# Kernel tuning notes

Measured on AMD Instinct MI355X. Metric: run time of the kernel, lower is better.

The kernel has to match this reference:

```python
import jax, jax.numpy as jnp
import numpy as np
import math

IN_DIM = 1024
OUT_DIM = 1024
GRID_SIZE = 5
SPLINE_ORDER = 3
N_COEFFS = GRID_SIZE + SPLINE_ORDER          # 8
N_KNOTS = GRID_SIZE + 2 * SPLINE_ORDER + 1   # 12
EPS = 1e-08


def setup_inputs() -> dict:
    key = jax.random.key(0)
    k_x, k_c, k_w = jax.random.split(key, 3)
    B = 4096
    x = jax.random.normal(k_x, (B, IN_DIM), dtype=jnp.float32)
    coeffs = jax.random.normal(k_c, (OUT_DIM, IN_DIM * N_COEFFS), dtype=jnp.float32) * 0.1
    # kaiming_uniform(a=sqrt(5)) -> U(-bound, bound), bound = sqrt(6/((1+a^2)*fan_in)) = 1/sqrt(fan_in)
    bound = 1.0 / math.sqrt(IN_DIM)
    base_weight = jax.random.uniform(k_w, (OUT_DIM, IN_DIM), dtype=jnp.float32,
                                     minval=-bound, maxval=bound)
    step = 2.0 / GRID_SIZE
    init_val = math.log(math.exp(step) - 1.0)
    grid_steps_log = jnp.full((IN_DIM, N_KNOTS - 1), init_val, dtype=jnp.float32)
    grid_start = jnp.full((IN_DIM, 1), -1.0 - SPLINE_ORDER * step, dtype=jnp.float32)
    res_scale = jnp.zeros((1,), dtype=jnp.float32)
    return {"x": x, "coeffs": coeffs, "base_weight": base_weight,
            "grid_steps_log": grid_steps_log, "grid_start": grid_start,
            "res_scale": res_scale}


def _get_grid(grid_steps_log, grid_start):
    steps = jax.nn.softplus(grid_steps_log)            # [in, n_knots-1]
    grid = jnp.concatenate([grid_start, steps], axis=-1)
    return jnp.cumsum(grid, axis=-1)                   # [in, n_knots]


def _b_spline(x, grid):
    # x: [B, in], grid: [in, n_knots] -> bases: [B, in, n_coeffs]
    x_u = x[:, :, None]                                # [B, in, 1]
    g = grid[None, :, :]                               # [1, in, n_knots]
    bases = ((x_u >= g[:, :, :-1]) & (x_u < g[:, :, 1:])).astype(x.dtype)
    for d in range(1, SPLINE_ORDER + 1):
        left = (x_u - g[:, :, :-(d + 1)]) / (g[:, :, d:-1] - g[:, :, :-(d + 1)] + EPS)
        right = (g[:, :, d + 1:] - x_u) / (g[:, :, d + 1:] - g[:, :, 1:-d] + EPS)
        bases = left * bases[:, :, :-1] + right * bases[:, :, 1:]
    return bases


def reference(x, coeffs, base_weight, grid_steps_log, grid_start, res_scale):
    grid = _get_grid(grid_steps_log, grid_start)
    spline_basis = _b_spline(x, grid)                  # [B, in, n_coeffs]
    B = spline_basis.shape[0]
    spline_flat = spline_basis.reshape(B, -1)          # [B, in*n_coeffs]
    spline_out = spline_flat @ coeffs.T                # [B, out]
    base_out = jax.nn.silu(x) @ base_weight.T          # [B, out]
    y = spline_out + base_out
    y = y + res_scale * x                              # residual (in_dim == out_dim)
    return y
```

## Files before the change

kernel.cpp:

```cpp
#include <hip/hip_runtime.h>

#define IN_DIM   1024
#define OUT_DIM  1024
#define BATCH    4096
#define NC       8
#define NK       12
#define KSPLINE  (IN_DIM * NC)
#define KDIM     (KSPLINE + IN_DIM)
#define EPS      1e-8f

#define NBLK_A   ((IN_DIM / 256) * (BATCH / 16))
#define NBLK_W   ((OUT_DIM * (KDIM / 4)) / 256)

#define BM       256
#define BN       128
#define BKQ      32
#define KSPLIT   2
#define KPS      (KDIM / KSPLIT)
#define NKT      (KPS / BKQ)
#define NGBLK    ((BATCH / BM) * (OUT_DIM / BN) * KSPLIT)

#define SWZ(r)   (((r) >> 1) & 3)

typedef _Float16 f16x8  __attribute__((ext_vector_type(8)));
typedef float    f32x4  __attribute__((ext_vector_type(4)));

static __device__ __forceinline__ unsigned short f2h_bits(float f) {
  _Float16 h = (_Float16)f;
  return __builtin_bit_cast(unsigned short, h);
}

static __device__ __forceinline__ void gl_lds16(const unsigned short* g, unsigned short* l) {
  __builtin_amdgcn_global_load_lds(
      (const __attribute__((address_space(1))) unsigned int*)g,
      (__attribute__((address_space(3))) unsigned int*)l, 16, 0, 0);
}

__global__ __launch_bounds__(256) void prep_k(const float* __restrict__ x,
                                              const float* __restrict__ coeffs,
                                              const float* __restrict__ bw,
                                              const float* __restrict__ gsl,
                                              const float* __restrict__ gstart,
                                              const float* __restrict__ rsp,
                                              unsigned short* __restrict__ A,
                                              unsigned short* __restrict__ W,
                                              float* __restrict__ out) {
  const int blk = blockIdx.x;
  if (blk < NBLK_A) {
    const int i  = (blk & 3) * 256 + threadIdx.x;
    const int b0 = (blk >> 2) * 16;
    const float rs = rsp[0];
    float g[NK];
    float acc = gstart[i];
    g[0] = acc;
#pragma unroll
    for (int t = 0; t < NK - 1; ++t) {
      float v  = gsl[i * (NK - 1) + t];
      float sp = (v > 20.f) ? v : log1pf(expf(v));
      acc += sp;
      g[t + 1] = acc;
    }
    float r[30];
#pragma unroll
    for (int j = 0; j < 11; ++j) r[j]      = 1.f / (g[j + 1] - g[j] + EPS);
#pragma unroll
    for (int j = 0; j < 10; ++j) r[11 + j] = 1.f / (g[j + 2] - g[j] + EPS);
#pragma unroll
    for (int j = 0; j <  9; ++j) r[21 + j] = 1.f / (g[j + 3] - g[j] + EPS);

#pragma unroll 4
    for (int bb = 0; bb < 16; ++bb) {
      const int b = b0 + bb;
      float xv = x[(size_t)b * IN_DIM + i];
      float bas[NK - 1];
#pragma unroll
      for (int k = 0; k < NK - 1; ++k)
        bas[k] = (xv >= g[k] && xv < g[k + 1]) ? 1.f : 0.f;
      const int off[3] = {0, 11, 21};
#pragma unroll
      for (int d = 1; d <= 3; ++d) {
#pragma unroll
        for (int k = 0; k < NK - 1 - d; ++k) {
          float left  = (xv - g[k])         * r[off[d - 1] + k];
          float right = (g[k + d + 1] - xv) * r[off[d - 1] + k + 1];
          bas[k] = left * bas[k] + right * bas[k + 1];
        }
      }
      uint4 pack;
      pack.x = (unsigned)f2h_bits(bas[0]) | ((unsigned)f2h_bits(bas[1]) << 16);
      pack.y = (unsigned)f2h_bits(bas[2]) | ((unsigned)f2h_bits(bas[3]) << 16);
      pack.z = (unsigned)f2h_bits(bas[4]) | ((unsigned)f2h_bits(bas[5]) << 16);
      pack.w = (unsigned)f2h_bits(bas[6]) | ((unsigned)f2h_bits(bas[7]) << 16);
      *(uint4*)&A[(size_t)b * KDIM + i * NC] = pack;
      float s = xv / (1.f + expf(-xv));
      A[(size_t)b * KDIM + KSPLINE + i] = f2h_bits(s);
      out[(size_t)b * OUT_DIM + i] = rs * xv;
    }
  } else {
    int idx = (blk - NBLK_A) * 256 + threadIdx.x;
    int n  = idx / (KDIM / 4);
    int k4 = (idx - n * (KDIM / 4)) * 4;
    float4 v;
    if (k4 < KSPLINE) v = *(const float4*)&coeffs[(size_t)n * KSPLINE + k4];
    else              v = *(const float4*)&bw[(size_t)n * IN_DIM + (k4 - KSPLINE)];
    ushort4 o;
    o.x = f2h_bits(v.x); o.y = f2h_bits(v.y); o.z = f2h_bits(v.z); o.w = f2h_bits(v.w);
    *(ushort4*)&W[(size_t)n * KDIM + k4] = o;
  }
}

__global__ __launch_bounds__(512, 2) void gemm_k(const unsigned short* __restrict__ A,
                                                 const unsigned short* __restrict__ W,
                                                 float* __restrict__ out,
                                                 float* __restrict__ P,
                                                 int use_partial) {
  __shared__ __align__(16) unsigned short As[4][BM][BKQ];
  __shared__ __align__(16) unsigned short Bs[4][BN][BKQ];
  const int tid  = threadIdx.x;
  const int wave = tid >> 6;
  const int lane = tid & 63;

  const int s  = (blockIdx.x & 7) * 32 + (blockIdx.x >> 3);
  const int ks = s >> 7;
  const int bn = (s >> 4) & 7;
  const int bm = s & 15;

  const int srow = tid >> 2;
  const int scsw = ((tid & 3) ^ SWZ(srow)) * 8;
  const unsigned short* aG = A + (size_t)(bm * BM + srow) * KDIM + (size_t)ks * KPS + scsw;
  const unsigned short* bG = W + (size_t)(bn * BN + srow) * KDIM + (size_t)ks * KPS + scsw;

#define STAGE(t) do {                                                          \
    const int sl_ = (t) & 3; const int kb_ = (t) * BKQ;                        \
    gl_lds16(aG + kb_,                      &As[sl_][wave * 16][0]);           \
    gl_lds16(aG + (size_t)128 * KDIM + kb_, &As[sl_][128 + wave * 16][0]);     \
    gl_lds16(bG + kb_,                      &Bs[sl_][wave * 16][0]);           \
  } while (0)

  const int l15 = lane & 15;
  const int kg  = lane >> 4;
  const int wm  = (wave >> 1) * 64;
  const int wn  = (wave & 1) * 64;

  f32x4 acc[4][4] = {};

  STAGE(0); STAGE(1); STAGE(2);
  asm volatile("s_waitcnt vmcnt(6)" ::: "memory");
  __builtin_amdgcn_s_barrier();

#pragma unroll 4
  for (int kt = 0; kt < NKT; ++kt) {
    const unsigned short* as = &As[kt & 3][0][0];
    const unsigned short* bs = &Bs[kt & 3][0][0];
    f16x8 af[4], bf[4];
#pragma unroll
    for (int mt = 0; mt < 4; ++mt) {
      int row = wm + mt * 16 + l15;
      af[mt] = *(const f16x8*)&as[row * BKQ + ((kg ^ SWZ(row)) * 8)];
    }
#pragma unroll
    for (int nt = 0; nt < 4; ++nt) {
      int row = wn + nt * 16 + l15;
      bf[nt] = *(const f16x8*)&bs[row * BKQ + ((kg ^ SWZ(row)) * 8)];
    }
    if (kt < NKT - 3) STAGE(kt + 3);
    __builtin_amdgcn_s_setprio(1);
#pragma unroll
    for (int mt = 0; mt < 4; ++mt)
#pragma unroll
      for (int nt = 0; nt < 4; ++nt)
        acc[mt][nt] = __builtin_amdgcn_mfma_f32_16x16x32_f16(af[mt], bf[nt], acc[mt][nt], 0, 0, 0);
    __builtin_amdgcn_s_setprio(0);
    if (kt < NKT - 3)       asm volatile("s_waitcnt vmcnt(6)" ::: "memory");
    else if (kt == NKT - 3) asm volatile("s_waitcnt vmcnt(3)" ::: "memory");
    else if (kt == NKT - 2) asm volatile("s_waitcnt vmcnt(0)" ::: "memory");
    if (kt < NKT - 1) __builtin_amdgcn_s_barrier();
  }
#undef STAGE

#pragma unroll
  for (int mt = 0; mt < 4; ++mt) {
#pragma unroll
    for (int reg = 0; reg < 4; ++reg) {
      const int row = bm * BM + wm + mt * 16 + kg * 4 + reg;
      const size_t ro = (size_t)row * OUT_DIM;
#pragma unroll
      for (int nt = 0; nt < 4; ++nt) {
        const int col = bn * BN + wn + nt * 16 + l15;
        const float v = acc[mt][nt][reg];
        if (use_partial) {
          if (ks == 0) out[ro + col] += v;
          else         P[ro + col]    = v;
        } else {
          atomicAdd(&out[ro + col], v);
        }
      }
    }
  }
}

__global__ __launch_bounds__(256) void reduce_k(float* __restrict__ out,
                                                const float* __restrict__ P) {
  const int n4 = (BATCH * OUT_DIM) / 4;
  for (int i = blockIdx.x * 256 + threadIdx.x; i < n4; i += gridDim.x * 256) {
    float4 o = ((const float4*)out)[i];
    float4 p = ((const float4*)P)[i];
    o.x += p.x; o.y += p.y; o.z += p.z; o.w += p.w;
    ((float4*)out)[i] = o;
  }
}

extern "C" void kernel_launch(void* const* d_in, const int* in_sizes, int n_in,
                              void* d_out, int out_size, void* d_ws, size_t ws_size,
                              hipStream_t stream) {
  const float* x      = (const float*)d_in[0];
  const float* coeffs = (const float*)d_in[1];
  const float* bw     = (const float*)d_in[2];
  const float* gsl    = (const float*)d_in[3];
  const float* gstart = (const float*)d_in[4];
  const float* rsp    = (const float*)d_in[5];

  const size_t szA = (size_t)BATCH * KDIM * 2;
  const size_t szW = (size_t)OUT_DIM * KDIM * 2;
  const size_t szP = (size_t)BATCH * OUT_DIM * 4;
  char* ws = (char*)d_ws;
  unsigned short* A  = (unsigned short*)ws;
  unsigned short* W  = (unsigned short*)(ws + szA);
  float*          P  = (float*)(ws + szA + szW);
  float*          out = (float*)d_out;
  const int use_partial = (ws_size >= szA + szW + szP) ? 1 : 0;

  prep_k<<<NBLK_A + NBLK_W, 256, 0, stream>>>(x, coeffs, bw, gsl, gstart, rsp, A, W, out);
  gemm_k<<<NGBLK, 512, 0, stream>>>(A, W, out, P, use_partial);
  if (use_partial) reduce_k<<<2048, 256, 0, stream>>>(out, P);
}
```

Baseline: 241.4 us.

## Restructure GEMM mainloop with BK=64, half-tile staging and interleaved MFMA phases

Doubles the K-tile to 64 and splits each A/B tile into half-tiles held in a 6-slot LDS ring. Each K step is broken into two phases, each running LDS fragment loads, prefetch of the next half-tiles and a batch of MFMAs, separated by barriers. The per-wave layout changes from a 64x64 wave tile to 128x32, and the XOR swizzle is widened to 8 chunks. Launch bounds drop to one block per CU, trading occupancy for a deeper, more finely interleaved load/compute pipeline. The loop runs in groups of three tiles, which assumes NKT is a multiple of three.

```diff
diff --git a/kernel.cpp b/kernel.cpp
--- a/kernel.cpp
+++ b/kernel.cpp
@@ -14,13 +14,13 @@
 
 #define BM       256
 #define BN       128
-#define BKQ      32
+#define BK       64
 #define KSPLIT   2
 #define KPS      (KDIM / KSPLIT)
-#define NKT      (KPS / BKQ)
+#define NKT      (KPS / BK)
 #define NGBLK    ((BATCH / BM) * (OUT_DIM / BN) * KSPLIT)
 
-#define SWZ(r)   (((r) >> 1) & 3)
+#define SWZ(r)   ((r) & 7)
 
 typedef _Float16 f16x8  __attribute__((ext_vector_type(8)));
 typedef float    f32x4  __attribute__((ext_vector_type(4)));
@@ -109,13 +109,13 @@
   }
 }
 
-__global__ __launch_bounds__(512, 2) void gemm_k(const unsigned short* __restrict__ A,
+__global__ __launch_bounds__(512, 1) void gemm_k(const unsigned short* __restrict__ A,
                                                  const unsigned short* __restrict__ W,
                                                  float* __restrict__ out,
                                                  float* __restrict__ P,
                                                  int use_partial) {
-  __shared__ __align__(16) unsigned short As[4][BM][BKQ];
-  __shared__ __align__(16) unsigned short Bs[4][BN][BKQ];
+  __shared__ __align__(16) unsigned short Al[6][128][64];
+  __shared__ __align__(16) unsigned short Bl[6][64][64];
   const int tid  = threadIdx.x;
   const int wave = tid >> 6;
   const int lane = tid & 63;
@@ -125,68 +125,112 @@
   const int bn = (s >> 4) & 7;
   const int bm = s & 15;
 
-  const int srow = tid >> 2;
-  const int scsw = ((tid & 3) ^ SWZ(srow)) * 8;
+  const int srow = tid >> 3;
+  const int scsw = ((tid & 7) ^ SWZ(srow)) * 8;
   const unsigned short* aG = A + (size_t)(bm * BM + srow) * KDIM + (size_t)ks * KPS + scsw;
   const unsigned short* bG = W + (size_t)(bn * BN + srow) * KDIM + (size_t)ks * KPS + scsw;
 
-#define STAGE(t) do {                                                          \
-    const int sl_ = (t) & 3; const int kb_ = (t) * BKQ;                        \
-    gl_lds16(aG + kb_,                      &As[sl_][wave * 16][0]);           \
-    gl_lds16(aG + (size_t)128 * KDIM + kb_, &As[sl_][128 + wave * 16][0]);     \
-    gl_lds16(bG + kb_,                      &Bs[sl_][wave * 16][0]);           \
+#define STAGE_A(u, sl, h) do {                                                 \
+    const size_t k_ = (size_t)(u) * BK;                                        \
+    gl_lds16(aG + ((size_t)(h) * 128)      * KDIM + k_, &Al[sl][wave * 8][0]); \
+    gl_lds16(aG + ((size_t)(h) * 128 + 64) * KDIM + k_, &Al[sl][64 + wave * 8][0]); \
   } while (0)
+#define STAGE_B(u, sl, h)                                                      \
+    gl_lds16(bG + ((size_t)(h) * 64) * KDIM + (size_t)(u) * BK, &Bl[sl][wave * 8][0])
 
   const int l15 = lane & 15;
   const int kg  = lane >> 4;
-  const int wm  = (wave >> 1) * 64;
-  const int wn  = (wave & 1) * 64;
-
-  f32x4 acc[4][4] = {};
-
-  STAGE(0); STAGE(1); STAGE(2);
+  const int wm  = (wave >> 2) * 128;
+  const int hA  = wave >> 2;
+  const int hB  = (wave & 3) >> 1;
+  const int wnl = (wave & 1) * 32;
+
+  f32x4 acc[8][2] = {};
+  f16x8 af[4][2], bf[2][2];
+
+  auto LDA = [&](const unsigned short (*As_)[64], int qm) {
+#pragma unroll
+    for (int i = 0; i < 4; ++i) {
+      const int rh = qm * 64 + i * 16 + l15;
+      const int sw = SWZ(rh);
+#pragma unroll
+      for (int kc = 0; kc < 2; ++kc)
+        af[i][kc] = *(const f16x8*)&As_[rh][((kc * 4 + kg) ^ sw) * 8];
+    }
+  };
+  auto LDB = [&](const unsigned short (*Bs_)[64]) {
+#pragma unroll
+    for (int j = 0; j < 2; ++j) {
+      const int rh = wnl + j * 16 + l15;
+      const int sw = SWZ(rh);
+#pragma unroll
+      for (int kc = 0; kc < 2; ++kc)
+        bf[j][kc] = *(const f16x8*)&Bs_[rh][((kc * 4 + kg) ^ sw) * 8];
+    }
+  };
+  auto MFMA_Q = [&](int m0) {
+#pragma unroll
+    for (int kc = 0; kc < 2; ++kc)
+#pragma unroll
+      for (int i = 0; i < 4; ++i)
+#pragma unroll
+        for (int j = 0; j < 2; ++j)
+          acc[m0 + i][j] = __builtin_amdgcn_mfma_f32_16x16x32_f16(af[i][kc], bf[j][kc], acc[m0 + i][j], 0, 0, 0);
+  };
+
+  STAGE_A(0, 0, 0); STAGE_B(0, 0, 0); STAGE_A(0, 1, 1); STAGE_B(0, 1, 1);
+  STAGE_A(1, 2, 0); STAGE_B(1, 2, 0); STAGE_A(1, 3, 1); STAGE_B(1, 3, 1);
   asm volatile("s_waitcnt vmcnt(6)" ::: "memory");
   __builtin_amdgcn_s_barrier();
 
-#pragma unroll 4
-  for (int kt = 0; kt < NKT; ++kt) {
-    const unsigned short* as = &As[kt & 3][0][0];
-    const unsigned short* bs = &Bs[kt & 3][0][0];
-    f16x8 af[4], bf[4];
-#pragma unroll
-    for (int mt = 0; mt < 4; ++mt) {
-      int row = wm + mt * 16 + l15;
-      af[mt] = *(const f16x8*)&as[row * BKQ + ((kg ^ SWZ(row)) * 8)];
-    }
-#pragma unroll
-    for (int nt = 0; nt < 4; ++nt) {
-      int row = wn + nt * 16 + l15;
-      bf[nt] = *(const f16x8*)&bs[row * BKQ + ((kg ^ SWZ(row)) * 8)];
-    }
-    if (kt < NKT - 3) STAGE(kt + 3);
-    __builtin_amdgcn_s_setprio(1);
-#pragma unroll
-    for (int mt = 0; mt < 4; ++mt)
-#pragma unroll
-      for (int nt = 0; nt < 4; ++nt)
-        acc[mt][nt] = __builtin_amdgcn_mfma_f32_16x16x32_f16(af[mt], bf[nt], acc[mt][nt], 0, 0, 0);
-    __builtin_amdgcn_s_setprio(0);
-    if (kt < NKT - 3)       asm volatile("s_waitcnt vmcnt(6)" ::: "memory");
-    else if (kt == NKT - 3) asm volatile("s_waitcnt vmcnt(3)" ::: "memory");
-    else if (kt == NKT - 2) asm volatile("s_waitcnt vmcnt(0)" ::: "memory");
-    if (kt < NKT - 1) __builtin_amdgcn_s_barrier();
-  }
-#undef STAGE
-
-#pragma unroll
-  for (int mt = 0; mt < 4; ++mt) {
+#define TILE(u, S0) do {                                                       \
+    const unsigned short (*As_)[64] = Al[(S0) + hA];                           \
+    const unsigned short (*Bs_)[64] = Bl[(S0) + hB];                           \
+                   \
+    LDA(As_, 0); LDB(Bs_);                                                     \
+    if ((u) + 2 < NKT) { STAGE_A((u) + 2, ((S0) + 4) % 6, 0);                  \
+                         STAGE_B((u) + 2, ((S0) + 4) % 6, 0); }                \
+    __builtin_amdgcn_s_barrier();                                              \
+    asm volatile("s_waitcnt lgkmcnt(0)" ::: "memory");                         \
+    __builtin_amdgcn_sched_barrier(0);                                         \
+    __builtin_amdgcn_s_setprio(1);                                             \
+    MFMA_Q(0);                                                                 \
+    __builtin_amdgcn_s_setprio(0);                                             \
+    __builtin_amdgcn_s_barrier();                                              \
+       \
+    LDA(As_, 1);                                                               \
+    if ((u) + 2 < NKT) { STAGE_A((u) + 2, ((S0) + 5) % 6, 1);                  \
+                         STAGE_B((u) + 2, ((S0) + 5) % 6, 1); }                \
+    __builtin_amdgcn_s_barrier();                                              \
+    asm volatile("s_waitcnt lgkmcnt(0)" ::: "memory");                         \
+    __builtin_amdgcn_sched_barrier(0);                                         \
+    __builtin_amdgcn_s_setprio(1);                                             \
+    MFMA_Q(4);                                                                 \
+    __builtin_amdgcn_s_setprio(0);                                             \
+         \
+    if ((u) < NKT - 2)       asm volatile("s_waitcnt vmcnt(6)" ::: "memory");  \
+    else if ((u) == NKT - 2) asm volatile("s_waitcnt vmcnt(0)" ::: "memory");  \
+    if ((u) < NKT - 1) __builtin_amdgcn_s_barrier();                           \
+  } while (0)
+
+  for (int uu = 0; uu < NKT; uu += 3) {
+    TILE(uu + 0, 0);
+    TILE(uu + 1, 2);
+    TILE(uu + 2, 4);
+  }
+#undef TILE
+#undef STAGE_A
+#undef STAGE_B
+
+#pragma unroll
+  for (int mt = 0; mt < 8; ++mt) {
 #pragma unroll
     for (int reg = 0; reg < 4; ++reg) {
       const int row = bm * BM + wm + mt * 16 + kg * 4 + reg;
       const size_t ro = (size_t)row * OUT_DIM;
 #pragma unroll
-      for (int nt = 0; nt < 4; ++nt) {
-        const int col = bn * BN + wn + nt * 16 + l15;
+      for (int nt = 0; nt < 2; ++nt) {
+        const int col = bn * BN + (wave & 3) * 32 + nt * 16 + l15;
         const float v = acc[mt][nt][reg];
         if (use_partial) {
           if (ks == 0) out[ro + col] += v;
```

Result: slower. 246.9 us (+2.3%).
